# Optimization experiments

Hardware: AMD Instinct MI355X
Metric: run time of the kernel (lower is better)

Reference implementation:

```python
import jax, jax.numpy as jnp
import numpy as np

TOPK = 2
RENORMALIZE = True

T, H, I, E = 2048, 2048, 5632, 8  # tokens, hidden, intermediate, experts


def setup_inputs() -> dict:
    key = jax.random.key(0)
    k1, k2, k3, k4 = jax.random.split(key, 4)
    x = jax.random.normal(k1, (T, H), dtype=jnp.float32)
    gating_output = jax.random.normal(k2, (T, E), dtype=jnp.float32)
    # gate_up_proj: concat of gate [E,I,H] and up [E,I,H] along dim 1 -> [E,2I,H]
    w1 = jax.random.normal(k3, (E, 2 * I, H), dtype=jnp.float32) * 0.02
    # down_proj: [E, H, I]
    w2 = jax.random.normal(k4, (E, H, I), dtype=jnp.float32) * 0.02
    return {"x": x, "gating_output": gating_output, "w1": w1, "w2": w2}


def _route(gating_output):
    # standard (non-grouped) top-k softmax routing, renormalized
    probs = jax.nn.softmax(gating_output, axis=-1)            # [T, E]
    topk_w, topk_idx = jax.lax.top_k(probs, TOPK)             # [T, K]
    if RENORMALIZE:
        topk_w = topk_w / jnp.sum(topk_w, axis=-1, keepdims=True)
    t = gating_output.shape[0]
    route = jnp.zeros((t, gating_output.shape[1]), dtype=topk_w.dtype)
    route = route.at[jnp.arange(t)[:, None], topk_idx].set(topk_w)  # [T, E]
    return route


def reference(x, gating_output, w1, w2):
    route = _route(gating_output)                             # [T, E]
    inter = w2.shape[-1]
    out = jnp.zeros_like(x)
    # loop over small fixed expert count; each iter is dense GEMM work
    for e in range(w1.shape[0]):
        gu = x @ w1[e].T                                      # [T, 2I]
        h = jax.nn.silu(gu[:, :inter]) * gu[:, inter:]        # SwiGLU  [T, I]
        out = out + (h @ w2[e].T) * route[:, e:e + 1]         # [T, H]
    return out
```

## Files before the change

### kernel.cpp

```cpp
#include <hip/hip_runtime.h>
#include <hip/hip_bf16.h>


#define TT 2048
#define HH 2048
#define II 5632
#define NE 8

using f32x4  = __attribute__((ext_vector_type(4))) float;
using bf16x8 = __attribute__((ext_vector_type(8))) short;

__device__ __forceinline__ uint32_t bfbits(float f) {
    __hip_bfloat16 h = __float2bfloat16(f);
    unsigned short u;
    __builtin_memcpy(&u, &h, 2);
    return (uint32_t)u;
}
__device__ __forceinline__ uint32_t pk2(float a, float b) {
    return bfbits(a) | (bfbits(b) << 16);
}
__device__ __forceinline__ uint4 pk8(const float4& a, const float4& b) {
    uint4 r;
    r.x = pk2(a.x, a.y); r.y = pk2(a.z, a.w);
    r.z = pk2(b.x, b.y); r.w = pk2(b.z, b.w);
    return r;
}
__device__ __forceinline__ void gl16(const void* g, void* l) {
    __builtin_amdgcn_global_load_lds(
        (const __attribute__((address_space(1))) unsigned int*)g,
        (__attribute__((address_space(3))) unsigned int*)l, 16, 0, 0);
}

__global__ void cvt_x(const float* __restrict__ x, __hip_bfloat16* __restrict__ xb) {
    const int i = (blockIdx.x * 256 + threadIdx.x) * 8;
    float4 a = *(const float4*)(x + i);
    float4 b = *(const float4*)(x + i + 4);
    *(uint4*)(xb + i) = pk8(a, b);
}

__global__ void route_topk(const float* __restrict__ gating,
                           int* __restrict__ tk_idx, float* __restrict__ tk_w) {
    int t = blockIdx.x * 256 + threadIdx.x;
    if (t >= TT) return;
    float g[NE];
#pragma unroll
    for (int e = 0; e < NE; e++) g[e] = gating[t * NE + e];
    int i0 = 0; float b0 = g[0];
#pragma unroll
    for (int e = 1; e < NE; e++) if (g[e] > b0) { b0 = g[e]; i0 = e; }
    int i1 = (i0 == 0) ? 1 : 0; float b1 = g[i1];
#pragma unroll
    for (int e = 0; e < NE; e++) if (e != i0 && g[e] > b1) { b1 = g[e]; i1 = e; }
    float ex = expf(b1 - b0);
    float w0 = 1.f / (1.f + ex);
    float w1 = ex / (1.f + ex);
    tk_idx[2 * t] = i0; tk_idx[2 * t + 1] = i1;
    tk_w[2 * t] = w0;  tk_w[2 * t + 1] = w1;
}

__global__ void build_lists(const int* __restrict__ tk_idx, const float* __restrict__ tk_w,
                            int* __restrict__ list_tok, float* __restrict__ list_w,
                            int* __restrict__ counts) {
    const int e = blockIdx.x;
    const int tid = threadIdx.x;
    int flag[8]; float wt[8];
    int cnt = 0;
#pragma unroll
    for (int j = 0; j < 8; j++) {
        int t = tid * 8 + j;
        int f = -1;
        if (tk_idx[2 * t] == e) f = 0;
        else if (tk_idx[2 * t + 1] == e) f = 1;
        flag[j] = f;
        wt[j] = (f >= 0) ? tk_w[2 * t + f] : 0.f;
        cnt += (f >= 0) ? 1 : 0;
    }
    __shared__ int s[256];
    s[tid] = cnt;
    __syncthreads();
    for (int d = 1; d < 256; d <<= 1) {
        int v = (tid >= d) ? s[tid - d] : 0;
        __syncthreads();
        s[tid] += v;
        __syncthreads();
    }
    int pos = s[tid] - cnt;
#pragma unroll
    for (int j = 0; j < 8; j++) {
        if (flag[j] >= 0) {
            list_tok[e * TT + pos] = tid * 8 + j;
            list_w[e * TT + pos] = wt[j];
            pos++;
        }
    }
    if (tid == 255) counts[e] = s[255];
}

__global__ __launch_bounds__(1024, 4) void gemm1_swiglu(
    const __hip_bfloat16* __restrict__ xb, const float* __restrict__ w1,
    const int* __restrict__ list_tok, const int* __restrict__ counts,
    __hip_bfloat16* __restrict__ hbuf) {
    const int e = blockIdx.y >> 3;
    const int mt = blockIdx.y & 7;
    const int cnt = counts[e];
    const int row0 = mt * 256;
    if (row0 >= cnt) return;
    int off = 0;
#pragma unroll
    for (int i = 0; i < NE; i++) if (i < e) off += counts[i];
    const int valid = min(256, cnt - row0);
    const int n0 = blockIdx.x * 128;
    const int tid = threadIdx.x;
    const int w = tid >> 6, l = tid & 63;

    __shared__ uint4 As[2 * 1024];
    __shared__ uint4 Bs[2 * 1024];

    const char* aSrc;
    {
        int r = w * 16 + (l >> 2);
        int t0 = list_tok[e * TT + row0 + min(r, valid - 1)];
        int s0 = (l & 3) ^ ((r >> 1) & 3);
        aSrc = (const char*)(xb + (size_t)t0 * HH + s0 * 8);
    }
    auto STAGEA = [&](int kt, int b) {
        gl16(aSrc + (size_t)kt * 64, (char*)As + b * 16384 + w * 1024);
    };

    const int br = tid >> 2, bu2 = tid & 3;
    const float* bSrc;
    {
        const float* base = w1 + (size_t)e * (2 * II) * HH;
        int r = (br < 128) ? (n0 + br) : (II + n0 + (br - 128));
        bSrc = base + (size_t)r * HH + bu2 * 8;
    }
    const int bwi = br * 4 + (bu2 ^ ((br >> 1) & 3));

    float4 rBa, rBb;
    auto LOADB = [&](int kt) {
        const int k = kt * 32;
        rBa = *(const float4*)(bSrc + k); rBb = *(const float4*)(bSrc + k + 4);
    };
    auto STOREB = [&](int b) { Bs[b * 1024 + bwi] = pk8(rBa, rBb); };

    const int wm = w >> 2, wn = w & 3;
    const int l15 = l & 15, ks = l >> 4;
    int aidx[4], bgidx[2], buidx[2];
#pragma unroll
    for (int m = 0; m < 4; m++) { int r = wm * 64 + m * 16 + l15; aidx[m] = r * 4 + (ks ^ ((r >> 1) & 3)); }
#pragma unroll
    for (int n = 0; n < 2; n++) {
        int cg = wn * 32 + n * 16 + l15;
        int cu = cg + 128;
        bgidx[n] = cg * 4 + (ks ^ ((cg >> 1) & 3));
        buidx[n] = cu * 4 + (ks ^ ((cu >> 1) & 3));
    }

    f32x4 accg[4][2], accu[4][2];
#pragma unroll
    for (int m = 0; m < 4; m++)
#pragma unroll
        for (int n = 0; n < 2; n++) { accg[m][n] = 0; accu[m][n] = 0; }

    STAGEA(0, 0); LOADB(0); STOREB(0);
    __syncthreads();
    const int KT = HH / 32;
#pragma unroll 2
    for (int kt = 0; kt < KT; ++kt) {
        const int cur = kt & 1;
        if (kt + 1 < KT) {
            STAGEA(kt + 1, cur ^ 1);
            LOADB(kt + 1);
        }
        bf16x8 gf[2], uf[2];
#pragma unroll
        for (int n = 0; n < 2; n++) {
            uint4 t = Bs[cur * 1024 + bgidx[n]]; gf[n] = __builtin_bit_cast(bf16x8, t);
            uint4 t2 = Bs[cur * 1024 + buidx[n]]; uf[n] = __builtin_bit_cast(bf16x8, t2);
        }
        const uint4* Ab = As + cur * 1024;
#pragma unroll
        for (int m = 0; m < 4; m++) {
            uint4 t = Ab[aidx[m]];
            bf16x8 af = __builtin_bit_cast(bf16x8, t);
#pragma unroll
            for (int n = 0; n < 2; n++) {
                accg[m][n] = __builtin_amdgcn_mfma_f32_16x16x32_bf16(af, gf[n], accg[m][n], 0, 0, 0);
                accu[m][n] = __builtin_amdgcn_mfma_f32_16x16x32_bf16(af, uf[n], accu[m][n], 0, 0, 0);
            }
        }
        if (kt + 1 < KT) STOREB(cur ^ 1);
        __syncthreads();
    }

#pragma unroll
    for (int m = 0; m < 4; m++) {
#pragma unroll
        for (int r = 0; r < 4; r++) {
            const int lr = wm * 64 + m * 16 + ks * 4 + r;
            if (lr < valid) {
                __hip_bfloat16* hrow = hbuf + (size_t)(off + row0 + lr) * II;
#pragma unroll
                for (int n = 0; n < 2; n++) {
                    const int col = n0 + wn * 32 + n * 16 + l15;
                    float g = accg[m][n][r], u = accu[m][n][r];
                    float h = g / (1.f + __expf(-g)) * u;
                    hrow[col] = __float2bfloat16(h);
                }
            }
        }
    }
}

__global__ __launch_bounds__(1024, 4) void gemm2_scatter(
    const __hip_bfloat16* __restrict__ hbuf, const float* __restrict__ w2,
    const int* __restrict__ list_tok, const float* __restrict__ list_w,
    const int* __restrict__ counts, float* __restrict__ out) {
    const int e = blockIdx.y >> 3;
    const int mt = blockIdx.y & 7;
    const int cnt = counts[e];
    const int row0 = mt * 256;
    if (row0 >= cnt) return;
    int off = 0;
#pragma unroll
    for (int i = 0; i < NE; i++) if (i < e) off += counts[i];
    const int valid = min(256, cnt - row0);
    const int n0 = blockIdx.x * 256;
    const int tid = threadIdx.x;
    const int w = tid >> 6, l = tid & 63;

    __shared__ uint4 As[2 * 1024];
    __shared__ uint4 Bs[2 * 1024];

    const char* aSrc;
    {
        int r = w * 16 + (l >> 2);
        int s0 = (l & 3) ^ ((r >> 1) & 3);
        aSrc = (const char*)(hbuf + (size_t)(off + row0 + min(r, valid - 1)) * II + s0 * 8);
    }
    auto STAGEA = [&](int kt, int b) {
        gl16(aSrc + (size_t)kt * 64, (char*)As + b * 16384 + w * 1024);
    };

    const int br = tid >> 2, bu2 = tid & 3;
    const float* bSrc = w2 + (size_t)e * HH * II + (size_t)(n0 + br) * II + bu2 * 8;
    const int bwi = br * 4 + (bu2 ^ ((br >> 1) & 3));

    float4 rBa, rBb;
    auto LOADB = [&](int kt) {
        const int k = kt * 32;
        rBa = *(const float4*)(bSrc + k); rBb = *(const float4*)(bSrc + k + 4);
    };
    auto STOREB = [&](int b) { Bs[b * 1024 + bwi] = pk8(rBa, rBb); };

    const int wm = w >> 2, wn = w & 3;
    const int l15 = l & 15, ks = l >> 4;
    int aidx[4], bidx[4];
#pragma unroll
    for (int m = 0; m < 4; m++) { int r = wm * 64 + m * 16 + l15; aidx[m] = r * 4 + (ks ^ ((r >> 1) & 3)); }
#pragma unroll
    for (int n = 0; n < 4; n++) { int c = wn * 64 + n * 16 + l15; bidx[n] = c * 4 + (ks ^ ((c >> 1) & 3)); }

    f32x4 acc[4][4];
#pragma unroll
    for (int m = 0; m < 4; m++)
#pragma unroll
        for (int n = 0; n < 4; n++) acc[m][n] = 0;

    STAGEA(0, 0); LOADB(0); STOREB(0);
    __syncthreads();
    const int KT = II / 32;
#pragma unroll 2
    for (int kt = 0; kt < KT; ++kt) {
        const int cur = kt & 1;
        if (kt + 1 < KT) {
            STAGEA(kt + 1, cur ^ 1);
            LOADB(kt + 1);
        }
        bf16x8 bf[4];
#pragma unroll
        for (int n = 0; n < 4; n++) { uint4 t = Bs[cur * 1024 + bidx[n]]; bf[n] = __builtin_bit_cast(bf16x8, t); }
        const uint4* Ab = As + cur * 1024;
#pragma unroll
        for (int m = 0; m < 4; m++) {
            uint4 t = Ab[aidx[m]];
            bf16x8 af = __builtin_bit_cast(bf16x8, t);
#pragma unroll
            for (int n = 0; n < 4; n++)
                acc[m][n] = __builtin_amdgcn_mfma_f32_16x16x32_bf16(af, bf[n], acc[m][n], 0, 0, 0);
        }
        if (kt + 1 < KT) STOREB(cur ^ 1);
        __syncthreads();
    }

#pragma unroll
    for (int m = 0; m < 4; m++) {
#pragma unroll
        for (int r = 0; r < 4; r++) {
            const int lr = wm * 64 + m * 16 + ks * 4 + r;
            if (lr < valid) {
                const int tok = list_tok[e * TT + row0 + lr];
                const float wt = list_w[e * TT + row0 + lr];
                float* orow = out + (size_t)tok * HH;
#pragma unroll
                for (int n = 0; n < 4; n++) {
                    const int col = n0 + wn * 64 + n * 16 + l15;
                    atomicAdd(orow + col, acc[m][n][r] * wt);
                }
            }
        }
    }
}

extern "C" void kernel_launch(void* const* d_in, const int* in_sizes, int n_in,
                              void* d_out, int out_size, void* d_ws, size_t ws_size,
                              hipStream_t stream) {
    const float* x      = (const float*)d_in[0];
    const float* gating = (const float*)d_in[1];
    const float* w1     = (const float*)d_in[2];
    const float* w2     = (const float*)d_in[3];
    float* out = (float*)d_out;
    char* ws = (char*)d_ws;

    int*   list_tok = (int*)(ws + 0);
    float* list_w   = (float*)(ws + (64 << 10));
    int*   counts   = (int*)(ws + (128 << 10));
    int*   tk_idx   = (int*)(ws + (132 << 10));
    float* tk_w     = (float*)(ws + (148 << 10));
    __hip_bfloat16* hbuf = (__hip_bfloat16*)(ws + (1 << 20));

    __hip_bfloat16* xb = (__hip_bfloat16*)d_out;

    route_topk<<<TT / 256, 256, 0, stream>>>(gating, tk_idx, tk_w);
    build_lists<<<NE, 256, 0, stream>>>(tk_idx, tk_w, list_tok, list_w, counts);
    cvt_x<<<TT * HH / (256 * 8), 256, 0, stream>>>(x, xb);
    gemm1_swiglu<<<dim3(II / 128, NE * 8), 1024, 0, stream>>>(xb, w1, list_tok, counts, hbuf);
    (void)hipMemsetAsync(d_out, 0, (size_t)TT * HH * sizeof(float), stream);
    gemm2_scatter<<<dim3(HH / 256, NE * 8), 1024, 0, stream>>>(hbuf, w2, list_tok, list_w, counts, out);
}
```

Measured before the change: 734.8 us.

## Stage fp32 weights directly into LDS with triple-buffered async pipeline

Both GEMM kernels now load the fp32 weight tiles straight into LDS with global_load_lds instead of going through registers, and convert them to bf16 only when reading fragments. The A/B buffers become a 3-deep ring with two tiles in flight, using explicit vmcnt waits and raw barriers in place of __syncthreads. This is meant to hide global-load latency and free registers used for staging. In exchange LDS use roughly doubles (fp32 B tiles, triple buffering), which can lower occupancy, and the fp32-to-bf16 conversion moves into the inner loop and is repeated by every wave that reads the same tile.

```diff
diff --git a/kernel.cpp b/kernel.cpp
--- a/kernel.cpp
+++ b/kernel.cpp
@@ -25,11 +25,19 @@
     r.z = pk2(b.x, b.y); r.w = pk2(b.z, b.w);
     return r;
 }
+__device__ __forceinline__ bf16x8 cvt8(const float4& a, const float4& b) {
+    uint4 t = pk8(a, b);
+    return __builtin_bit_cast(bf16x8, t);
+}
 __device__ __forceinline__ void gl16(const void* g, void* l) {
     __builtin_amdgcn_global_load_lds(
         (const __attribute__((address_space(1))) unsigned int*)g,
         (__attribute__((address_space(3))) unsigned int*)l, 16, 0, 0);
 }
+
+#define VMW3() asm volatile("s_waitcnt vmcnt(3)" ::: "memory")
+#define VMW0() asm volatile("s_waitcnt vmcnt(0)" ::: "memory")
+#define BARR() __builtin_amdgcn_s_barrier()
 
 __global__ void cvt_x(const float* __restrict__ x, __hip_bfloat16* __restrict__ xb) {
     const int i = (blockIdx.x * 256 + threadIdx.x) * 8;
@@ -113,8 +121,8 @@
     const int tid = threadIdx.x;
     const int w = tid >> 6, l = tid & 63;
 
-    __shared__ uint4 As[2 * 1024];
-    __shared__ uint4 Bs[2 * 1024];
+    __shared__ uint4 As[3 * 1024];
+    __shared__ uint4 Bs[3 * 2048];
 
     const char* aSrc;
     {
@@ -123,37 +131,37 @@
         int s0 = (l & 3) ^ ((r >> 1) & 3);
         aSrc = (const char*)(xb + (size_t)t0 * HH + s0 * 8);
     }
-    auto STAGEA = [&](int kt, int b) {
-        gl16(aSrc + (size_t)kt * 64, (char*)As + b * 16384 + w * 1024);
+    const char *bSrc0, *bSrc1;
+    {
+        int r0 = tid >> 3, p0 = tid & 7;
+        int l0 = p0 ^ (r0 & 7);
+        const float* base = w1 + (size_t)e * (2 * II) * HH;
+        bSrc0 = (const char*)(base + (size_t)(n0 + r0) * HH + l0 * 4);
+        bSrc1 = (const char*)(base + (size_t)(II + n0 + r0) * HH + l0 * 4);
+    }
+    auto STAGE = [&](int kt, int b) {
+        const size_t kA = (size_t)kt * 64;
+        const size_t kB = (size_t)kt * 128;
+        gl16(aSrc + kA, (char*)As + b * 16384 + w * 1024);
+        gl16(bSrc0 + kB, (char*)Bs + b * 32768 + w * 1024);
+        gl16(bSrc1 + kB, (char*)Bs + b * 32768 + 16384 + w * 1024);
     };
-
-    const int br = tid >> 2, bu2 = tid & 3;
-    const float* bSrc;
-    {
-        const float* base = w1 + (size_t)e * (2 * II) * HH;
-        int r = (br < 128) ? (n0 + br) : (II + n0 + (br - 128));
-        bSrc = base + (size_t)r * HH + bu2 * 8;
-    }
-    const int bwi = br * 4 + (bu2 ^ ((br >> 1) & 3));
-
-    float4 rBa, rBb;
-    auto LOADB = [&](int kt) {
-        const int k = kt * 32;
-        rBa = *(const float4*)(bSrc + k); rBb = *(const float4*)(bSrc + k + 4);
-    };
-    auto STOREB = [&](int b) { Bs[b * 1024 + bwi] = pk8(rBa, rBb); };
 
     const int wm = w >> 2, wn = w & 3;
     const int l15 = l & 15, ks = l >> 4;
-    int aidx[4], bgidx[2], buidx[2];
+    int aidx[4];
 #pragma unroll
     for (int m = 0; m < 4; m++) { int r = wm * 64 + m * 16 + l15; aidx[m] = r * 4 + (ks ^ ((r >> 1) & 3)); }
+    int bg0[2], bg1[2], bu0[2], bu1[2];
 #pragma unroll
     for (int n = 0; n < 2; n++) {
         int cg = wn * 32 + n * 16 + l15;
         int cu = cg + 128;
-        bgidx[n] = cg * 4 + (ks ^ ((cg >> 1) & 3));
-        buidx[n] = cu * 4 + (ks ^ ((cu >> 1) & 3));
+        int x7 = cg & 7;
+        bg0[n] = cg * 8 + ((2 * ks) ^ x7);
+        bg1[n] = cg * 8 + ((2 * ks + 1) ^ x7);
+        bu0[n] = cu * 8 + ((2 * ks) ^ x7);
+        bu1[n] = cu * 8 + ((2 * ks + 1) ^ x7);
     }
 
     f32x4 accg[4][2], accu[4][2];
@@ -162,23 +170,22 @@
 #pragma unroll
         for (int n = 0; n < 2; n++) { accg[m][n] = 0; accu[m][n] = 0; }
 
-    STAGEA(0, 0); LOADB(0); STOREB(0);
-    __syncthreads();
     const int KT = HH / 32;
-#pragma unroll 2
+    STAGE(0, 0); STAGE(1, 1);
+    VMW3();
+    BARR();
+
     for (int kt = 0; kt < KT; ++kt) {
-        const int cur = kt & 1;
-        if (kt + 1 < KT) {
-            STAGEA(kt + 1, cur ^ 1);
-            LOADB(kt + 1);
-        }
+        const int b = kt % 3;
+        if (kt + 2 < KT) { int b2 = (kt + 2) % 3; STAGE(kt + 2, b2); }
+        const float4* Bb = (const float4*)Bs + b * 2048;
         bf16x8 gf[2], uf[2];
 #pragma unroll
         for (int n = 0; n < 2; n++) {
-            uint4 t = Bs[cur * 1024 + bgidx[n]]; gf[n] = __builtin_bit_cast(bf16x8, t);
-            uint4 t2 = Bs[cur * 1024 + buidx[n]]; uf[n] = __builtin_bit_cast(bf16x8, t2);
-        }
-        const uint4* Ab = As + cur * 1024;
+            gf[n] = cvt8(Bb[bg0[n]], Bb[bg1[n]]);
+            uf[n] = cvt8(Bb[bu0[n]], Bb[bu1[n]]);
+        }
+        const uint4* Ab = As + b * 1024;
 #pragma unroll
         for (int m = 0; m < 4; m++) {
             uint4 t = Ab[aidx[m]];
@@ -189,8 +196,10 @@
                 accu[m][n] = __builtin_amdgcn_mfma_f32_16x16x32_bf16(af, uf[n], accu[m][n], 0, 0, 0);
             }
         }
-        if (kt + 1 < KT) STOREB(cur ^ 1);
-        __syncthreads();
+        if (kt + 1 < KT) {
+            if (kt + 2 < KT) VMW3(); else VMW0();
+            BARR();
+        }
     }
 
 #pragma unroll
@@ -229,8 +238,8 @@
     const int tid = threadIdx.x;
     const int w = tid >> 6, l = tid & 63;
 
-    __shared__ uint4 As[2 * 1024];
-    __shared__ uint4 Bs[2 * 1024];
+    __shared__ uint4 As[3 * 1024];
+    __shared__ uint4 Bs[3 * 2048];
 
     const char* aSrc;
     {
@@ -238,28 +247,35 @@
         int s0 = (l & 3) ^ ((r >> 1) & 3);
         aSrc = (const char*)(hbuf + (size_t)(off + row0 + min(r, valid - 1)) * II + s0 * 8);
     }
-    auto STAGEA = [&](int kt, int b) {
-        gl16(aSrc + (size_t)kt * 64, (char*)As + b * 16384 + w * 1024);
+    const char *bSrc0, *bSrc1;
+    {
+        int r0 = tid >> 3, p0 = tid & 7;
+        int l0 = p0 ^ (r0 & 7);
+        const float* base = w2 + (size_t)e * HH * II;
+        bSrc0 = (const char*)(base + (size_t)(n0 + r0) * II + l0 * 4);
+        bSrc1 = (const char*)(base + (size_t)(n0 + r0 + 128) * II + l0 * 4);
+    }
+    auto STAGE = [&](int kt, int b) {
+        const size_t kA = (size_t)kt * 64;
+        const size_t kB = (size_t)kt * 128;
+        gl16(aSrc + kA, (char*)As + b * 16384 + w * 1024);
+        gl16(bSrc0 + kB, (char*)Bs + b * 32768 + w * 1024);
+        gl16(bSrc1 + kB, (char*)Bs + b * 32768 + 16384 + w * 1024);
     };
-
-    const int br = tid >> 2, bu2 = tid & 3;
-    const float* bSrc = w2 + (size_t)e * HH * II + (size_t)(n0 + br) * II + bu2 * 8;
-    const int bwi = br * 4 + (bu2 ^ ((br >> 1) & 3));
-
-    float4 rBa, rBb;
-    auto LOADB = [&](int kt) {
-        const int k = kt * 32;
-        rBa = *(const float4*)(bSrc + k); rBb = *(const float4*)(bSrc + k + 4);
-    };
-    auto STOREB = [&](int b) { Bs[b * 1024 + bwi] = pk8(rBa, rBb); };
 
     const int wm = w >> 2, wn = w & 3;
     const int l15 = l & 15, ks = l >> 4;
-    int aidx[4], bidx[4];
+    int aidx[4];
 #pragma unroll
     for (int m = 0; m < 4; m++) { int r = wm * 64 + m * 16 + l15; aidx[m] = r * 4 + (ks ^ ((r >> 1) & 3)); }
-#pragma unroll
-    for (int n = 0; n < 4; n++) { int c = wn * 64 + n * 16 + l15; bidx[n] = c * 4 + (ks ^ ((c >> 1) & 3)); }
+    int b0i[4], b1i[4];
+#pragma unroll
+    for (int n = 0; n < 4; n++) {
+        int c = wn * 64 + n * 16 + l15;
+        int x7 = c & 7;
+        b0i[n] = c * 8 + ((2 * ks) ^ x7);
+        b1i[n] = c * 8 + ((2 * ks + 1) ^ x7);
+    }
 
     f32x4 acc[4][4];
 #pragma unroll
@@ -267,20 +283,19 @@
 #pragma unroll
         for (int n = 0; n < 4; n++) acc[m][n] = 0;
 
-    STAGEA(0, 0); LOADB(0); STOREB(0);
-    __syncthreads();
     const int KT = II / 32;
-#pragma unroll 2
+    STAGE(0, 0); STAGE(1, 1);
+    VMW3();
+    BARR();
+
     for (int kt = 0; kt < KT; ++kt) {
-        const int cur = kt & 1;
-        if (kt + 1 < KT) {
-            STAGEA(kt + 1, cur ^ 1);
-            LOADB(kt + 1);
-        }
+        const int b = kt % 3;
+        if (kt + 2 < KT) { int b2 = (kt + 2) % 3; STAGE(kt + 2, b2); }
+        const float4* Bb = (const float4*)Bs + b * 2048;
         bf16x8 bf[4];
 #pragma unroll
-        for (int n = 0; n < 4; n++) { uint4 t = Bs[cur * 1024 + bidx[n]]; bf[n] = __builtin_bit_cast(bf16x8, t); }
-        const uint4* Ab = As + cur * 1024;
+        for (int n = 0; n < 4; n++) bf[n] = cvt8(Bb[b0i[n]], Bb[b1i[n]]);
+        const uint4* Ab = As + b * 1024;
 #pragma unroll
         for (int m = 0; m < 4; m++) {
             uint4 t = Ab[aidx[m]];
@@ -289,8 +304,10 @@
             for (int n = 0; n < 4; n++)
                 acc[m][n] = __builtin_amdgcn_mfma_f32_16x16x32_bf16(af, bf[n], acc[m][n], 0, 0, 0);
         }
-        if (kt + 1 < KT) STOREB(cur ^ 1);
-        __syncthreads();
+        if (kt + 1 < KT) {
+            if (kt + 2 < KT) VMW3(); else VMW0();
+            BARR();
+        }
     }
 
 #pragma unroll
```

New measurement: 924.7 us. +25.9%, slower.
